# Kernel tuning notes

Hardware: AMD Instinct MI355X
Metric: run time of the kernel (lower is better)

## Reference

```python
import jax, jax.numpy as jnp
import numpy as np

IN_FEATURES = 128
OUT_FEATURES = 64

def setup_inputs() -> dict:
    key = jax.random.key(0)
    k1, k2, k3 = jax.random.split(key, 3)
    x = jax.random.normal(k1, (8, 4096, IN_FEATURES), dtype=jnp.float32)
    # nn.Linear weights: W [out, in], a [1, 2*out]
    W = jax.random.normal(k2, (OUT_FEATURES, IN_FEATURES), dtype=jnp.float32) / np.sqrt(IN_FEATURES)
    a = jax.random.normal(k3, (1, 2 * OUT_FEATURES), dtype=jnp.float32) / np.sqrt(2 * OUT_FEATURES)
    return {"x": x, "W": W, "a": a}

def reference(x, W, a):
    # h = x @ W.T : [B, N, D]
    h = jnp.einsum('bnf,df->bnd', x, W)
    d = h.shape[-1]
    a1 = a[0, :d]  # [D]
    a2 = a[0, d:]  # [D]
    score1 = h @ a1  # [B, N]
    score2 = h @ a2  # [B, N]
    # outer-sum broadcast: e[b,i,j] = leakyrelu(score1[b,i] + score2[b,j])
    e = jax.nn.leaky_relu(score1[:, :, None] + score2[:, None, :], negative_slope=0.2)
    attention = jax.nn.softmax(e, axis=-1)  # [B, N, N]
    h_prime = jnp.einsum('bij,bjd->bid', attention, h)
    return jax.nn.elu(h_prime)
```

## Files before the change

### kernel.cpp

```cpp
#include <hip/hip_runtime.h>
#include <hip/hip_bf16.h>

#define BB 8
#define NN 4096
#define FF 128
#define DD 64
#define NB (BB*NN)
#define CHK 128
#define NCH (NN/CHK)
#define CSZ 16
#define NC16 (NN/CSZ)
#define CH 72

#define OFF_H     0
#define OFF_S1    (OFF_H    + (size_t)NB*DD*4)
#define OFF_S2    (OFF_S1   + (size_t)NB*4)
#define OFF_S2S   (OFF_S2   + (size_t)NB*4)
#define OFF_PK    (OFF_S2S  + (size_t)NB*4)
#define OFF_CT16  (OFF_PK   + (size_t)NB*8)
#define OFF_CTS   (OFF_CT16 + (size_t)BB*NC16*2*CH*8)
#define OFF_PRANK (OFF_CTS  + (size_t)BB*(NC16+1)*2*CH*8)

__device__ __forceinline__ unsigned int fkey(float f) {
  unsigned int u = __float_as_uint(f);
  return (u & 0x80000000u) ? ~u : (u | 0x80000000u);
}

__global__ __launch_bounds__(256) void gat_kA(const float* __restrict__ x,
                                              const float* __restrict__ W,
                                              const float* __restrict__ a,
                                              float* __restrict__ h,
                                              float* __restrict__ s1,
                                              float* __restrict__ s2) {
  __shared__ float xs[64][FF];
  const int tid  = threadIdx.x;
  const int lane = tid & 63;
  const int wave = tid >> 6;
  const long long rowbase = (long long)blockIdx.x * 64;

  const float4* x4  = (const float4*)(x + rowbase * FF);
  float4*       xs4 = (float4*)&xs[0][0];
#pragma unroll
  for (int i = 0; i < 8; ++i) xs4[tid + i * 256] = x4[tid + i * 256];

  float4 wreg[32];
  const float4* W4 = (const float4*)(W + lane * FF);
#pragma unroll
  for (int j = 0; j < 32; ++j) wreg[j] = W4[j];
  const float a1d = a[lane];
  const float a2d = a[DD + lane];
  __syncthreads();

#pragma unroll 2
  for (int r = wave * 16; r < wave * 16 + 16; ++r) {
    const float4* xr = (const float4*)&xs[r][0];
    float4 acc = {0.f, 0.f, 0.f, 0.f};
#pragma unroll
    for (int j = 0; j < 32; ++j) {
      float4 xv = xr[j];
      acc.x += xv.x * wreg[j].x;
      acc.y += xv.y * wreg[j].y;
      acc.z += xv.z * wreg[j].z;
      acc.w += xv.w * wreg[j].w;
    }
    float hd = (acc.x + acc.y) + (acc.z + acc.w);
    const long long row = rowbase + r;
    h[row * DD + lane] = hd;

    float p1 = hd * a1d, p2 = hd * a2d;
#pragma unroll
    for (int o = 32; o; o >>= 1) { p1 += __shfl_xor(p1, o); p2 += __shfl_xor(p2, o); }
    if (lane == 0) { s1[row] = p1; s2[row] = p2; }
  }
}

__global__ __launch_bounds__(256) void gat_kB1(const float* __restrict__ s2,
                                               unsigned short* __restrict__ prank) {
  __shared__ unsigned long long ks[CHK];
  const int c = blockIdx.x, b = blockIdx.y, tid = threadIdx.x;
  const float* s2b = s2 + (size_t)b * NN;

  if (tid < CHK) {
    const int ig = c * CHK + tid;
    ks[tid] = ((unsigned long long)fkey(s2b[ig]) << 12) | (unsigned)ig;
  }

  unsigned long long kj[16];
  int rank[16];
#pragma unroll
  for (int t = 0; t < 16; ++t) {
    const int j = tid + 256 * t;
    kj[t] = ((unsigned long long)fkey(s2b[j]) << 12) | (unsigned)j;
    rank[t] = 0;
  }
  __syncthreads();

#pragma unroll 4
  for (int i = 0; i < CHK; ++i) {
    const unsigned long long ki = ks[i];
#pragma unroll
    for (int t = 0; t < 16; ++t) rank[t] += (ki < kj[t]) ? 1 : 0;
  }

  unsigned short* pr = prank + ((size_t)c * BB + b) * NN;
#pragma unroll
  for (int t = 0; t < 16; ++t) pr[tid + 256 * t] = (unsigned short)rank[t];
}

__global__ __launch_bounds__(256) void gat_kB2(const float* __restrict__ s2,
                                               const unsigned short* __restrict__ prank,
                                               float* __restrict__ s2s,
                                               int2* __restrict__ pk) {
  __shared__ float red[4];
  const int b = blockIdx.y, tid = threadIdx.x;
  const int j = blockIdx.x * 256 + tid;
  const float* s2b = s2 + (size_t)b * NN;

  float mx = -3.4e38f;
  for (int i = tid; i < NN; i += 256) mx = fmaxf(mx, s2b[i]);
#pragma unroll
  for (int o = 32; o; o >>= 1) mx = fmaxf(mx, __shfl_xor(mx, o));
  if ((tid & 63) == 0) red[tid >> 6] = mx;
  __syncthreads();
  mx = fmaxf(fmaxf(red[0], red[1]), fmaxf(red[2], red[3]));

  int rank = 0;
#pragma unroll 8
  for (int c = 0; c < NCH; ++c) rank += prank[((size_t)c * BB + b) * NN + j];

  const float key = s2b[j];
  const float wn = expf(0.2f * (key - mx));
  const size_t o = (size_t)b * NN + rank;
  s2s[o] = key;
  pk[o]  = make_int2(j, __float_as_int(wn));
}

__global__ __launch_bounds__(64) void gat_kC(const float* __restrict__ h,
                                             const int2* __restrict__ pk,
                                             double* __restrict__ CT16) {
  const int c = blockIdx.x, b = blockIdx.y, d = threadIdx.x;
  const int base = b * NN + c * CSZ;
  double ap = 0, an = 0, zp = 0, zn = 0;
#pragma unroll
  for (int s = 0; s < CSZ; ++s) {
    const int2 p = pk[base + s];
    const float hv = h[((size_t)(b * NN + p.x)) * DD + d];
    const float wn = __int_as_float(p.y);
    const float w2 = wn * wn;
    const float wp = w2 * w2 * wn;
    an += (double)wn * hv; ap += (double)wp * hv;
    zn += wn;              zp += wp;
  }
  double* o = CT16 + ((size_t)(b * NC16 + c) * 2) * CH;
  o[0 * CH + d] = an;
  o[1 * CH + d] = ap;
  if (d == 0) { o[0 * CH + 64] = zn; o[1 * CH + 64] = zp; }
}

__global__ __launch_bounds__(128) void gat_kD(const double* __restrict__ CT16,
                                              double* __restrict__ CTS) {
  const int b = blockIdx.x, fam = blockIdx.y, ch = threadIdx.x;
  if (ch > 64) return;
  double off = 0;
#pragma unroll 16
  for (int c = 0; c < NC16; ++c) {
    CTS[(((size_t)b * (NC16 + 1) + c) * 2 + fam) * CH + ch] = off;
    off += CT16[(((size_t)b * NC16 + c) * 2 + fam) * CH + ch];
  }
  CTS[(((size_t)b * (NC16 + 1) + NC16) * 2 + fam) * CH + ch] = off;
}

__global__ __launch_bounds__(256) void gat_kF(const float* __restrict__ s1,
                                              const float* __restrict__ s2s,
                                              const int2* __restrict__ pk,
                                              const float* __restrict__ h,
                                              const double* __restrict__ CTS,
                                              float* __restrict__ out) {
  __shared__ float key[NN];
  __shared__ float seglast[64];
  const int b = blockIdx.y;
  const int tid = threadIdx.x, lane = tid & 63, wv = tid >> 6;

  const float4* src = (const float4*)(s2s + (size_t)b * NN);
  float4* dst = (float4*)key;
#pragma unroll
  for (int i = 0; i < 4; ++i) dst[tid + 256 * i] = src[tid + 256 * i];
  __syncthreads();
  if (tid < 64) seglast[tid] = key[tid * 64 + 63];
  __syncthreads();

  const int bNN = b * NN;
  const float c1 = key[NN - 1];
  const double* base0 = CTS + ((size_t)b * (NC16 + 1)) * 2 * CH;
  const double* tt = base0 + (size_t)NC16 * 2 * CH + CH;
  const double tot = tt[lane];
  const double Zt  = tt[64];
  const float segl = seglast[lane];

  const int row0 = blockIdx.x * 32 + wv * 8;
  float s1v[8];
#pragma unroll
  for (int r = 0; r < 8; ++r) s1v[r] = s1[bNN + row0 + r];

#pragma unroll 2
  for (int r = 0; r < 8; ++r) {
    const int rowl = row0 + r;
    const float s1i = s1v[r];
    const float t = -s1i;

    unsigned long long m1 = __ballot(segl <= t);
    int seg = __popcll(m1); if (seg > 63) seg = 63;
    const float v2 = key[seg * 64 + lane];
    const int k = seg * 64 + __popcll(__ballot(v2 <= t));
    const int c16 = k >> 4, cnt = k & 15;

    const bool up   = (cnt <= 8);
    const int  cb   = up ? c16 : c16 + 1;
    const int  nref = up ? cnt : 16 - cnt;
    const int  j0   = up ? (c16 << 4) : k;
    const float sgn = up ? 1.0f : -1.0f;

    const double* r0 = base0 + (size_t)cb * 2 * CH;
    const double* r1 = r0 + CH;
    double pre  = r0[lane];
    double p1v  = r1[lane];
    double Zpre = r0[64];
    double Z1   = r1[64];

#pragma unroll
    for (int jj = 0; jj < 8; ++jj) {
      int jn = j0 + jj; jn = jn < NN ? jn : NN - 1;
      const int2 p = pk[bNN + jn];
      const float hv = h[((size_t)(bNN + p.x)) * DD + lane];
      const float msk = (jj < nref) ? sgn : 0.0f;
      const float w  = __int_as_float(p.y) * msk;
      const float w2 = w * w;
      const float wp = w2 * w2 * w;
      pre += (double)w * hv; p1v += (double)wp * hv;
      Zpre += w;             Z1  += wp;
    }

    const float suf_d = (float)(tot - p1v);
    const float Zsuf  = (float)(Zt - Z1);
    const float z = s1i + c1;
    const float m = z >= 0.f ? z : 0.2f * z;
    const float A  = expf(z - m);
    const float Bn = expf(0.2f * z - m);
    const float num = A * suf_d + Bn * (float)pre;
    const float Z   = A * Zsuf  + Bn * (float)Zpre;
    const float hp  = num / Z;
    out[((size_t)(bNN + rowl)) * DD + lane] = hp > 0.f ? hp : expm1f(hp);
  }
}

extern "C" void kernel_launch(void* const* d_in, const int* in_sizes, int n_in,
                              void* d_out, int out_size, void* d_ws, size_t ws_size,
                              hipStream_t stream) {
  const float* x = (const float*)d_in[0];
  const float* W = (const float*)d_in[1];
  const float* a = (const float*)d_in[2];
  float* out = (float*)d_out;

  char* ws = (char*)d_ws;
  float*  h    = (float*)(ws + OFF_H);
  float*  s1   = (float*)(ws + OFF_S1);
  float*  s2   = (float*)(ws + OFF_S2);
  float*  s2s  = (float*)(ws + OFF_S2S);
  int2*   pk   = (int2*) (ws + OFF_PK);
  double* CT16 = (double*)(ws + OFF_CT16);
  double* CTS  = (double*)(ws + OFF_CTS);
  unsigned short* prank = (unsigned short*)(ws + OFF_PRANK);

  gat_kA<<<NB / 64, 256, 0, stream>>>(x, W, a, h, s1, s2);
  gat_kB1<<<dim3(NCH, BB), 256, 0, stream>>>(s2, prank);
  gat_kB2<<<dim3(NN / 256, BB), 256, 0, stream>>>(s2, prank, s2s, pk);
  gat_kC<<<dim3(NC16, BB), 64, 0, stream>>>(h, pk, CT16);
  gat_kD<<<dim3(BB, 2), 128, 0, stream>>>(CT16, CTS);
  gat_kF<<<dim3(NN / 32, BB), 256, 0, stream>>>(s1, s2s, pk, h, CTS, out);
}
```

Before: 81.73 us.

## Fuse prefix-scan into chunk kernel via last-block atomic, precompute score max in sort

Removes the separate kD scan launch: each kC block bumps a per-batch done counter, and the last block to finish runs the prefix scan over the chunk totals. The per-batch max of score2 is now computed in kB1 with an atomicMax on order-preserving keys, so kB2 no longer scans all 4096 values per block. The intent is to save one launch and the redundant max reductions. In exchange it adds atomics and fences and makes the scan run serially inside one block per batch.

```diff
diff --git a/kernel.cpp b/kernel.cpp
--- a/kernel.cpp
+++ b/kernel.cpp
@@ -20,10 +20,15 @@
 #define OFF_CT16  (OFF_PK   + (size_t)NB*8)
 #define OFF_CTS   (OFF_CT16 + (size_t)BB*NC16*2*CH*8)
 #define OFF_PRANK (OFF_CTS  + (size_t)BB*(NC16+1)*2*CH*8)
+#define OFF_DONE  (OFF_PRANK + (size_t)NCH*BB*NN*2)
+#define OFF_BMAX  (OFF_DONE  + 64)
 
 __device__ __forceinline__ unsigned int fkey(float f) {
   unsigned int u = __float_as_uint(f);
   return (u & 0x80000000u) ? ~u : (u | 0x80000000u);
+}
+__device__ __forceinline__ float inv_fkey(unsigned int u) {
+  return (u & 0x80000000u) ? __uint_as_float(u ^ 0x80000000u) : __uint_as_float(~u);
 }
 
 __global__ __launch_bounds__(256) void gat_kA(const float* __restrict__ x,
@@ -31,12 +36,15 @@
                                               const float* __restrict__ a,
                                               float* __restrict__ h,
                                               float* __restrict__ s1,
-                                              float* __restrict__ s2) {
+                                              float* __restrict__ s2,
+                                              unsigned int* __restrict__ bmax) {
   __shared__ float xs[64][FF];
   const int tid  = threadIdx.x;
   const int lane = tid & 63;
   const int wave = tid >> 6;
   const long long rowbase = (long long)blockIdx.x * 64;
+
+  if ((blockIdx.x & 63) == 0 && tid == 0) bmax[blockIdx.x >> 6] = 0u;
 
   const float4* x4  = (const float4*)(x + rowbase * FF);
   float4*       xs4 = (float4*)&xs[0][0];
@@ -75,11 +83,15 @@
 }
 
 __global__ __launch_bounds__(256) void gat_kB1(const float* __restrict__ s2,
-                                               unsigned short* __restrict__ prank) {
+                                               unsigned short* __restrict__ prank,
+                                               unsigned int* __restrict__ bmax,
+                                               unsigned int* __restrict__ done) {
   __shared__ unsigned long long ks[CHK];
   const int c = blockIdx.x, b = blockIdx.y, tid = threadIdx.x;
   const float* s2b = s2 + (size_t)b * NN;
 
+  if (c == 0 && b == 0 && tid < BB) done[tid] = 0u;
+
   if (tid < CHK) {
     const int ig = c * CHK + tid;
     ks[tid] = ((unsigned long long)fkey(s2b[ig]) << 12) | (unsigned)ig;
@@ -87,11 +99,14 @@
 
   unsigned long long kj[16];
   int rank[16];
+  unsigned int fmax = 0u;
 #pragma unroll
   for (int t = 0; t < 16; ++t) {
     const int j = tid + 256 * t;
-    kj[t] = ((unsigned long long)fkey(s2b[j]) << 12) | (unsigned)j;
+    const unsigned int fk = fkey(s2b[j]);
+    kj[t] = ((unsigned long long)fk << 12) | (unsigned)j;
     rank[t] = 0;
+    fmax = fmax > fk ? fmax : fk;
   }
   __syncthreads();
 
@@ -102,6 +117,13 @@
     for (int t = 0; t < 16; ++t) rank[t] += (ki < kj[t]) ? 1 : 0;
   }
 
+#pragma unroll
+  for (int o = 32; o; o >>= 1) {
+    unsigned int v = __shfl_xor(fmax, o);
+    fmax = fmax > v ? fmax : v;
+  }
+  if ((tid & 63) == 0) atomicMax(&bmax[b], fmax);
+
   unsigned short* pr = prank + ((size_t)c * BB + b) * NN;
 #pragma unroll
   for (int t = 0; t < 16; ++t) pr[tid + 256 * t] = (unsigned short)rank[t];
@@ -109,20 +131,13 @@
 
 __global__ __launch_bounds__(256) void gat_kB2(const float* __restrict__ s2,
                                                const unsigned short* __restrict__ prank,
+                                               const unsigned int* __restrict__ bmax,
                                                float* __restrict__ s2s,
                                                int2* __restrict__ pk) {
-  __shared__ float red[4];
   const int b = blockIdx.y, tid = threadIdx.x;
   const int j = blockIdx.x * 256 + tid;
   const float* s2b = s2 + (size_t)b * NN;
-
-  float mx = -3.4e38f;
-  for (int i = tid; i < NN; i += 256) mx = fmaxf(mx, s2b[i]);
-#pragma unroll
-  for (int o = 32; o; o >>= 1) mx = fmaxf(mx, __shfl_xor(mx, o));
-  if ((tid & 63) == 0) red[tid >> 6] = mx;
-  __syncthreads();
-  mx = fmaxf(fmaxf(red[0], red[1]), fmaxf(red[2], red[3]));
+  const float mx = inv_fkey(bmax[b]);
 
   int rank = 0;
 #pragma unroll 8
@@ -135,39 +150,54 @@
   pk[o]  = make_int2(j, __float_as_int(wn));
 }
 
-__global__ __launch_bounds__(64) void gat_kC(const float* __restrict__ h,
-                                             const int2* __restrict__ pk,
-                                             double* __restrict__ CT16) {
-  const int c = blockIdx.x, b = blockIdx.y, d = threadIdx.x;
-  const int base = b * NN + c * CSZ;
-  double ap = 0, an = 0, zp = 0, zn = 0;
-#pragma unroll
-  for (int s = 0; s < CSZ; ++s) {
-    const int2 p = pk[base + s];
-    const float hv = h[((size_t)(b * NN + p.x)) * DD + d];
-    const float wn = __int_as_float(p.y);
-    const float w2 = wn * wn;
-    const float wp = w2 * w2 * wn;
-    an += (double)wn * hv; ap += (double)wp * hv;
-    zn += wn;              zp += wp;
-  }
-  double* o = CT16 + ((size_t)(b * NC16 + c) * 2) * CH;
-  o[0 * CH + d] = an;
-  o[1 * CH + d] = ap;
-  if (d == 0) { o[0 * CH + 64] = zn; o[1 * CH + 64] = zp; }
-}
-
-__global__ __launch_bounds__(128) void gat_kD(const double* __restrict__ CT16,
-                                              double* __restrict__ CTS) {
-  const int b = blockIdx.x, fam = blockIdx.y, ch = threadIdx.x;
-  if (ch > 64) return;
-  double off = 0;
+__global__ __launch_bounds__(128) void gat_kC(const float* __restrict__ h,
+                                              const int2* __restrict__ pk,
+                                              double* __restrict__ CT16,
+                                              double* __restrict__ CTS,
+                                              unsigned int* __restrict__ done) {
+  __shared__ int isLast;
+  const int c = blockIdx.x, b = blockIdx.y, tid = threadIdx.x;
+
+  if (tid < 64) {
+    const int d = tid;
+    const int base = b * NN + c * CSZ;
+    double ap = 0, an = 0, zp = 0, zn = 0;
+#pragma unroll
+    for (int s = 0; s < CSZ; ++s) {
+      const int2 p = pk[base + s];
+      const float hv = h[((size_t)(b * NN + p.x)) * DD + d];
+      const float wn = __int_as_float(p.y);
+      const float w2 = wn * wn;
+      const float wp = w2 * w2 * wn;
+      an += (double)wn * hv; ap += (double)wp * hv;
+      zn += wn;              zp += wp;
+    }
+    double* o = CT16 + ((size_t)(b * NC16 + c) * 2) * CH;
+    o[0 * CH + d] = an;
+    o[1 * CH + d] = ap;
+    if (d == 0) { o[0 * CH + 64] = zn; o[1 * CH + 64] = zp; }
+  }
+
+  __threadfence();
+  __syncthreads();
+  if (tid == 0) {
+    const unsigned int old = atomicAdd(&done[b], 1u);
+    isLast = (old == (unsigned)(NC16 - 1)) ? 1 : 0;
+  }
+  __syncthreads();
+  if (!isLast) return;
+
+  __threadfence();
+  for (int s = tid; s < 130; s += 128) {
+    const int fam = s / 65, ch = s % 65;
+    double off = 0;
 #pragma unroll 16
-  for (int c = 0; c < NC16; ++c) {
-    CTS[(((size_t)b * (NC16 + 1) + c) * 2 + fam) * CH + ch] = off;
-    off += CT16[(((size_t)b * NC16 + c) * 2 + fam) * CH + ch];
-  }
-  CTS[(((size_t)b * (NC16 + 1) + NC16) * 2 + fam) * CH + ch] = off;
+    for (int cc = 0; cc < NC16; ++cc) {
+      CTS[(((size_t)b * (NC16 + 1) + cc) * 2 + fam) * CH + ch] = off;
+      off += CT16[(((size_t)b * NC16 + cc) * 2 + fam) * CH + ch];
+    }
+    CTS[(((size_t)b * (NC16 + 1) + NC16) * 2 + fam) * CH + ch] = off;
+  }
 }
 
 __global__ __launch_bounds__(256) void gat_kF(const float* __restrict__ s1,
@@ -270,11 +300,12 @@
   double* CT16 = (double*)(ws + OFF_CT16);
   double* CTS  = (double*)(ws + OFF_CTS);
   unsigned short* prank = (unsigned short*)(ws + OFF_PRANK);
-
-  gat_kA<<<NB / 64, 256, 0, stream>>>(x, W, a, h, s1, s2);
-  gat_kB1<<<dim3(NCH, BB), 256, 0, stream>>>(s2, prank);
-  gat_kB2<<<dim3(NN / 256, BB), 256, 0, stream>>>(s2, prank, s2s, pk);
-  gat_kC<<<dim3(NC16, BB), 64, 0, stream>>>(h, pk, CT16);
-  gat_kD<<<dim3(BB, 2), 128, 0, stream>>>(CT16, CTS);
+  unsigned int*   done  = (unsigned int*)(ws + OFF_DONE);
+  unsigned int*   bmax  = (unsigned int*)(ws + OFF_BMAX);
+
+  gat_kA<<<NB / 64, 256, 0, stream>>>(x, W, a, h, s1, s2, bmax);
+  gat_kB1<<<dim3(NCH, BB), 256, 0, stream>>>(s2, prank, bmax, done);
+  gat_kB2<<<dim3(NN / 256, BB), 256, 0, stream>>>(s2, prank, bmax, s2s, pk);
+  gat_kC<<<dim3(NC16, BB), 128, 0, stream>>>(h, pk, CT16, CTS, done);
   gat_kF<<<dim3(NN / 32, BB), 256, 0, stream>>>(s1, s2s, pk, h, CTS, out);
 }
```

Result: slower. 187.6 us (+129.5%).
